# Optimization experiments

Hardware: AMD Instinct MI355X
Metric: run time of the kernel (lower is better)

Reference implementation:

```python
import jax, jax.numpy as jnp
import numpy as np

CLOUD_CLUSTER_NUM = 4
CLOUD_NODE_NUM = 32
EDGE_NODE_NUM = 64
FAILC = -100.0
D_BB = 768            # 256*3 backbone features
D_IN = D_BB + 5 * 5 * 6  # 918, fc1 input
D_H = 128


def setup_inputs() -> dict:
    key = jax.random.key(0)
    ks = jax.random.split(key, 18)
    C, t = 64, 64
    s = 0.05
    return {
        "clusternum": C,
        "tasknum": t,
        "backbone_y": jax.random.normal(ks[0], (C, t, D_BB), jnp.float32),
        "y_res": jax.random.uniform(ks[1], (C, t, 5), jnp.float32),
        "y_fr": jax.random.uniform(ks[2], (C, t, 5), jnp.float32),
        "y_estep": jax.random.uniform(ks[3], (C, t, 6), jnp.float32),
        "y_enode": jax.random.uniform(ks[4], (C, t, EDGE_NODE_NUM), jnp.float32),
        "y_ccluster": jax.random.uniform(ks[5], (C, t, CLOUD_CLUSTER_NUM), jnp.float32),
        "y_cnode": jax.random.uniform(ks[6], (C, t, CLOUD_NODE_NUM), jnp.float32),
        "W1": jax.random.normal(ks[7], (D_IN, D_H), jnp.float32) * s,
        "b1": jnp.zeros((D_H,), jnp.float32),
        "W3": jax.random.normal(ks[8], (D_H, 1), jnp.float32) * s,
        "b3": jnp.zeros((1,), jnp.float32),
        "W4": jax.random.normal(ks[9], (D_H, 1), jnp.float32) * s,
        "b4": jnp.zeros((1,), jnp.float32),
        "W5": jax.random.normal(ks[10], (D_H, 1), jnp.float32) * s,
        "b5": jnp.zeros((1,), jnp.float32),
        "W6": jax.random.normal(ks[11], (D_H, 1), jnp.float32) * s,
        "b6": jnp.zeros((1,), jnp.float32),
    }


def reference(clusternum, tasknum, backbone_y, y_res, y_fr, y_estep, y_enode,
              y_ccluster, y_cnode, W1, b1, W3, b3, W4, b4, W5, b5, W6, b6):
    # All per-cluster ops in the original loop are row-wise per task, so the
    # uniform ragged batch flattens to T = clusternum * tasknum tasks.
    T = clusternum * tasknum
    bb = backbone_y.reshape(T, D_BB)
    res = y_res.reshape(T, 5)
    fr = y_fr.reshape(T, 5)
    estep = y_estep.reshape(T, 6)
    enode = y_enode.reshape(T, EDGE_NODE_NUM)
    ccl = y_ccluster.reshape(T, CLOUD_CLUSTER_NUM)
    cnd = y_cnode.reshape(T, CLOUD_NODE_NUM)

    # outer product cluster x node -> flattened cloud-node features [T, 128]
    y_cnodes = jnp.einsum('jn,jm->jnm', ccl, cnd).reshape(T, CLOUD_NODE_NUM * CLOUD_CLUSTER_NUM)
    # 3-way outer product [T,5,5,6] -> [T,150], concat with backbone -> fc1 + relu
    y2 = jnp.einsum('jn,jm,jo->jnmo', res, fr, estep).reshape(T, 5 * 5 * 6)
    y2 = jnp.concatenate([y2, bb], axis=1)
    y2 = jax.nn.relu(y2 @ W1 + b1)  # [T, 128]

    y31 = jnp.einsum('jk,jl->jlk', y2, enode)     # [T, E, 128]
    y32 = jnp.einsum('jk,jl->jlk', y2, y_cnodes)  # [T, 128, 128]
    y41 = jnp.mean(y31, axis=1)  # [T, 128]
    y42 = jnp.sum(y32, axis=1)   # [T, 128]

    y51 = jax.nn.sigmoid((y41 @ W3 + b3)[:, 0])  # [T]
    y61 = (y41 @ W4 + b4)[:, 0]                  # [T]
    y52 = jax.nn.sigmoid((y42 @ W5 + b5)[:, 0])  # [T]
    y62 = (y42 @ W6 + b6)[:, 0]                  # [T]

    # torch broadcasting: [T] * [1,T] -> [1,T] (elementwise)
    p = y51 * y52
    y = (1.0 - p) * FAILC + p * (y61 + y62)
    return y[None, :]  # [1, T]
```

## Files before the change

kernel.cpp:

```cpp
#include <hip/hip_runtime.h>
#include <hip/hip_bf16.h>


typedef __bf16  bf16x8 __attribute__((ext_vector_type(8)));
typedef float   f32x4  __attribute__((ext_vector_type(4)));
typedef unsigned int uintx4 __attribute__((ext_vector_type(4)));
typedef unsigned short ushort4e __attribute__((ext_vector_type(4)));

#define FAILC -100.0f
#define ASTRIDE 936

static __device__ __forceinline__ unsigned short f2bf(float f) {
    unsigned u = __builtin_bit_cast(unsigned, f);
    u = (u + 0x7FFFu + ((u >> 16) & 1u)) >> 16;
    return (unsigned short)u;
}

__global__ __launch_bounds__(512) void critic_fused(
    const float* __restrict__ bb,
    const float* __restrict__ res,
    const float* __restrict__ fr,
    const float* __restrict__ estep,
    const float* __restrict__ enode,
    const float* __restrict__ ccl,
    const float* __restrict__ cnd,
    const float* __restrict__ W1,
    const float* __restrict__ b1,
    const float* __restrict__ W3, const float* __restrict__ b3,
    const float* __restrict__ W4, const float* __restrict__ b4,
    const float* __restrict__ W5, const float* __restrict__ b5,
    const float* __restrict__ W6, const float* __restrict__ b6,
    float* __restrict__ out)
{
    __shared__ unsigned short a_lds[16 * ASTRIDE];
    __shared__ float s_y2[16][132];
    __shared__ float s_small[16][16];

    const int t = threadIdx.x;
    const int task0 = blockIdx.x * 16;

    const int lane = t & 63;
    const int wave = t >> 6;
    const int mrow = lane & 15;
    const int quad = lane >> 4;
    const int ncol = wave * 16 + mrow;

    const float4* bbp = (const float4*)(bb + (size_t)task0 * 768);
    float4 bbv[6];
#pragma unroll
    for (int it = 0; it < 6; ++it) bbv[it] = bbp[t + it * 512];

    if (t < 256) {
        int r = t >> 4, q = t & 15;
        int tg = task0 + r;
        float v;
        if (q < 5)       v = res[tg * 5 + q];
        else if (q < 10) v = fr[tg * 5 + (q - 5)];
        else             v = estep[tg * 6 + (q - 10)];
        s_small[r][q] = v;
    }

    uintx4 barr[29];
#pragma unroll
    for (int c = 0; c < 29; ++c) {
        const int kq0 = c * 32 + quad * 8;
        float fv[8];
#pragma unroll
        for (int j = 0; j < 8; ++j) {
            int k = kq0 + j;
            int row = (k < 768) ? (150 + k) : (k - 768);
            fv[j] = (k < 918) ? W1[(size_t)row * 128 + ncol] : 0.0f;
        }
        uintx4 bp;
        bp.x = (unsigned)f2bf(fv[0]) | ((unsigned)f2bf(fv[1]) << 16);
        bp.y = (unsigned)f2bf(fv[2]) | ((unsigned)f2bf(fv[3]) << 16);
        bp.z = (unsigned)f2bf(fv[4]) | ((unsigned)f2bf(fv[5]) << 16);
        bp.w = (unsigned)f2bf(fv[6]) | ((unsigned)f2bf(fv[7]) << 16);
        barr[c] = bp;
    }

#pragma unroll
    for (int it = 0; it < 6; ++it) {
        int i = t + it * 512;
        int m = i / 192;
        int off = (i - m * 192) * 4;
        float4 v = bbv[it];
        ushort4e pk = { f2bf(v.x), f2bf(v.y), f2bf(v.z), f2bf(v.w) };
        *(ushort4e*)&a_lds[m * ASTRIDE + off] = pk;
    }
    __syncthreads();

    for (int w = t; w < 2560; w += 512) {
        if (w < 2400) {
            int r = w / 150;
            int idx = w - r * 150;
            int n = idx / 30;
            int rem = idx - n * 30;
            int m = rem / 6;
            int o = rem - m * 6;
            float v = s_small[r][n] * s_small[r][5 + m] * s_small[r][10 + o];
            a_lds[r * ASTRIDE + 768 + idx] = f2bf(v);
        } else {
            int z = w - 2400;
            int r = z / 10;
            a_lds[r * ASTRIDE + 918 + (z - r * 10)] = 0;
        }
    }
    __syncthreads();

    const unsigned short* aptr = a_lds + mrow * ASTRIDE + quad * 8;

    f32x4 acc = {0.f, 0.f, 0.f, 0.f};
#pragma unroll
    for (int c = 0; c < 29; ++c) {
        uintx4 au = *(const uintx4*)(aptr + c * 32);
        acc = __builtin_amdgcn_mfma_f32_16x16x32_bf16(
            __builtin_bit_cast(bf16x8, au), __builtin_bit_cast(bf16x8, barr[c]),
            acc, 0, 0, 0);
    }

    {
        float bias = b1[ncol];
#pragma unroll
        for (int r = 0; r < 4; ++r) {
            int m = quad * 4 + r;
            s_y2[m][ncol] = fmaxf(acc[r] + bias, 0.f);
        }
    }
    __syncthreads();

    const int kq = t & 31;
    const int rsub = t >> 5;
    const int tg = task0 + rsub;
    const int k4 = kq * 4;

    float4 yv = *(const float4*)&s_y2[rsub][k4];
    float y0 = yv.x, y1 = yv.y, y2v = yv.z, y3 = yv.w;

    float4 w3v = *(const float4*)(W3 + k4);
    float4 w4v = *(const float4*)(W4 + k4);
    float4 w5v = *(const float4*)(W5 + k4);
    float4 w6v = *(const float4*)(W6 + k4);
    float pd3 = y0 * w3v.x + y1 * w3v.y + y2v * w3v.z + y3 * w3v.w;
    float pd4 = y0 * w4v.x + y1 * w4v.y + y2v * w4v.z + y3 * w4v.w;
    float pd5 = y0 * w5v.x + y1 * w5v.y + y2v * w5v.z + y3 * w5v.w;
    float pd6 = y0 * w6v.x + y1 * w6v.y + y2v * w6v.z + y3 * w6v.w;

    const float* en = enode + (size_t)tg * 64 + kq * 2;
    float pe = en[0] + en[1];
    float pc = (kq < 4) ? ccl[tg * 4 + kq] : 0.f;
    float pn = cnd[tg * 32 + kq];

#pragma unroll
    for (int m = 1; m < 32; m <<= 1) {
        pd3 += __shfl_xor(pd3, m);
        pd4 += __shfl_xor(pd4, m);
        pd5 += __shfl_xor(pd5, m);
        pd6 += __shfl_xor(pd6, m);
        pe  += __shfl_xor(pe, m);
        pc  += __shfl_xor(pc, m);
        pn  += __shfl_xor(pn, m);
    }

    if (kq == 0) {
        float me = pe * (1.0f / 64.0f);
        float sc = pc * pn;
        float a3 = me * pd3 + b3[0];
        float a5 = sc * pd5 + b5[0];
        float y51 = 1.0f / (1.0f + __expf(-a3));
        float y52 = 1.0f / (1.0f + __expf(-a5));
        float y61 = me * pd4 + b4[0];
        float y62 = sc * pd6 + b6[0];
        float p = y51 * y52;
        out[tg] = (1.0f - p) * FAILC + p * (y61 + y62);
    }
}

extern "C" void kernel_launch(void* const* d_in, const int* in_sizes, int n_in,
                              void* d_out, int out_size, void* d_ws, size_t ws_size,
                              hipStream_t stream) {
    const float* bb    = (const float*)d_in[2];
    const float* res   = (const float*)d_in[3];
    const float* fr    = (const float*)d_in[4];
    const float* estep = (const float*)d_in[5];
    const float* enode = (const float*)d_in[6];
    const float* ccl   = (const float*)d_in[7];
    const float* cnd   = (const float*)d_in[8];
    const float* W1    = (const float*)d_in[9];
    const float* b1    = (const float*)d_in[10];
    const float* W3    = (const float*)d_in[11];
    const float* b3    = (const float*)d_in[12];
    const float* W4    = (const float*)d_in[13];
    const float* b4    = (const float*)d_in[14];
    const float* W5    = (const float*)d_in[15];
    const float* b5    = (const float*)d_in[16];
    const float* W6    = (const float*)d_in[17];
    const float* b6    = (const float*)d_in[18];
    float* out = (float*)d_out;

    int T = in_sizes[3] / 5;
    int blocks = T / 16;

    hipLaunchKernelGGL(critic_fused, dim3(blocks), dim3(512), 0, stream,
                       bb, res, fr, estep, enode, ccl, cnd,
                       W1, b1, W3, b3, W4, b4, W5, b5, W6, b6, out);
}
```

Measured before the change: 113.3 us.

## Stream W1 loads through a 4-slot register pipeline and drop s_small staging

The 29-chunk W1 load-and-convert that used to fill all B fragments up front is replaced by a rolling 4-slot register buffer, prefetched 3 chunks ahead inside the MFMA loop. This cuts register pressure and lets the weight loads overlap the matrix multiply. The res/fr/estep values are now loaded straight into registers per output element instead of going through shared memory, which removes one __syncthreads. In exchange, each thread issues redundant small global loads, and the W1 load latency now sits on the MFMA loop's critical path.

```diff
diff --git a/kernel.cpp b/kernel.cpp
--- a/kernel.cpp
+++ b/kernel.cpp
@@ -34,7 +34,6 @@
 {
     __shared__ unsigned short a_lds[16 * ASTRIDE];
     __shared__ float s_y2[16][132];
-    __shared__ float s_small[16][16];
 
     const int t = threadIdx.x;
     const int task0 = blockIdx.x * 16;
@@ -50,33 +49,22 @@
 #pragma unroll
     for (int it = 0; it < 6; ++it) bbv[it] = bbp[t + it * 512];
 
-    if (t < 256) {
-        int r = t >> 4, q = t & 15;
-        int tg = task0 + r;
-        float v;
-        if (q < 5)       v = res[tg * 5 + q];
-        else if (q < 10) v = fr[tg * 5 + (q - 5)];
-        else             v = estep[tg * 6 + (q - 10)];
-        s_small[r][q] = v;
-    }
-
-    uintx4 barr[29];
-#pragma unroll
-    for (int c = 0; c < 29; ++c) {
-        const int kq0 = c * 32 + quad * 8;
-        float fv[8];
-#pragma unroll
-        for (int j = 0; j < 8; ++j) {
-            int k = kq0 + j;
-            int row = (k < 768) ? (150 + k) : (k - 768);
-            fv[j] = (k < 918) ? W1[(size_t)row * 128 + ncol] : 0.0f;
-        }
-        uintx4 bp;
-        bp.x = (unsigned)f2bf(fv[0]) | ((unsigned)f2bf(fv[1]) << 16);
-        bp.y = (unsigned)f2bf(fv[2]) | ((unsigned)f2bf(fv[3]) << 16);
-        bp.z = (unsigned)f2bf(fv[4]) | ((unsigned)f2bf(fv[5]) << 16);
-        bp.w = (unsigned)f2bf(fv[6]) | ((unsigned)f2bf(fv[7]) << 16);
-        barr[c] = bp;
+    float ov0[5], ov1[5], ov2[5];
+#pragma unroll
+    for (int it = 0; it < 5; ++it) {
+        int w = t + it * 512;
+        if (w < 2400) {
+            int r = w / 150;
+            int idx = w - r * 150;
+            int n = idx / 30;
+            int rem = idx - n * 30;
+            int m = rem / 6;
+            int o = rem - m * 6;
+            int tg = task0 + r;
+            ov0[it] = res[tg * 5 + n];
+            ov1[it] = fr[tg * 5 + m];
+            ov2[it] = estep[tg * 6 + o];
+        }
     }
 
 #pragma unroll
@@ -88,17 +76,14 @@
         ushort4e pk = { f2bf(v.x), f2bf(v.y), f2bf(v.z), f2bf(v.w) };
         *(ushort4e*)&a_lds[m * ASTRIDE + off] = pk;
     }
-    __syncthreads();
-
-    for (int w = t; w < 2560; w += 512) {
+
+#pragma unroll
+    for (int it = 0; it < 5; ++it) {
+        int w = t + it * 512;
         if (w < 2400) {
             int r = w / 150;
             int idx = w - r * 150;
-            int n = idx / 30;
-            int rem = idx - n * 30;
-            int m = rem / 6;
-            int o = rem - m * 6;
-            float v = s_small[r][n] * s_small[r][5 + m] * s_small[r][10 + o];
+            float v = ov0[it] * ov1[it] * ov2[it];
             a_lds[r * ASTRIDE + 768 + idx] = f2bf(v);
         } else {
             int z = w - 2400;
@@ -110,12 +95,41 @@
 
     const unsigned short* aptr = a_lds + mrow * ASTRIDE + quad * 8;
 
+    float bw[4][8];
+#pragma unroll
+    for (int c = 0; c < 3; ++c) {
+        const int kq0 = c * 32 + quad * 8;
+#pragma unroll
+        for (int j = 0; j < 8; ++j) {
+            int k = kq0 + j;
+            int row = (k < 768) ? (150 + k) : (k - 768);
+            bw[c][j] = (k < 918) ? W1[(size_t)row * 128 + ncol] : 0.0f;
+        }
+    }
+
     f32x4 acc = {0.f, 0.f, 0.f, 0.f};
 #pragma unroll
     for (int c = 0; c < 29; ++c) {
+        const int slot = c & 3;
+        uintx4 bp;
+        bp.x = (unsigned)f2bf(bw[slot][0]) | ((unsigned)f2bf(bw[slot][1]) << 16);
+        bp.y = (unsigned)f2bf(bw[slot][2]) | ((unsigned)f2bf(bw[slot][3]) << 16);
+        bp.z = (unsigned)f2bf(bw[slot][4]) | ((unsigned)f2bf(bw[slot][5]) << 16);
+        bp.w = (unsigned)f2bf(bw[slot][6]) | ((unsigned)f2bf(bw[slot][7]) << 16);
+        if (c + 3 < 29) {
+            const int cn = c + 3;
+            const int sn = cn & 3;
+            const int kq0 = cn * 32 + quad * 8;
+#pragma unroll
+            for (int j = 0; j < 8; ++j) {
+                int k = kq0 + j;
+                int row = (k < 768) ? (150 + k) : (k - 768);
+                bw[sn][j] = (k < 918) ? W1[(size_t)row * 128 + ncol] : 0.0f;
+            }
+        }
         uintx4 au = *(const uintx4*)(aptr + c * 32);
         acc = __builtin_amdgcn_mfma_f32_16x16x32_bf16(
-            __builtin_bit_cast(bf16x8, au), __builtin_bit_cast(bf16x8, barr[c]),
+            __builtin_bit_cast(bf16x8, au), __builtin_bit_cast(bf16x8, bp),
             acc, 0, 0, 0);
     }
 
```

Result: faster. 107.5 us (-5.1%).
